# Kernel tuning notes

Measured on AMD Instinct MI355X. Metric: run time of the kernel, lower is better.

Reference implementation:

```python
import jax, jax.numpy as jnp
import numpy as np

S, B, H, NH = 2048, 1, 4096, 32
HD = H // NH            # 128
ROT = int(HD * 0.25)    # 32 partial rotary dims
BASE = 10000.0


def setup_inputs() -> dict:
    key = jax.random.key(0)
    ks = jax.random.split(key, 4)
    hidden_states = jax.random.normal(ks[0], (S, B, H), dtype=jnp.float32)
    W_qkv = jax.random.normal(ks[1], (3 * H, H), dtype=jnp.float32) * 0.02
    b_qkv = jnp.zeros((3 * H,), dtype=jnp.float32)
    W_dense = jax.random.normal(ks[2], (H, H), dtype=jnp.float32) * 0.02
    b_dense = jnp.zeros((H,), dtype=jnp.float32)
    # causal left-to-right mask, True = attend
    attention_mask = jnp.tril(jnp.ones((S, S), dtype=bool))[None, None]  # [1,1,S,S]
    return dict(hidden_states=hidden_states, attention_mask=attention_mask,
                W_qkv=W_qkv, b_qkv=b_qkv, W_dense=W_dense, b_dense=b_dense)


def _rotate_half(x):
    x1, x2 = jnp.split(x, 2, axis=-1)
    return jnp.concatenate((-x2, x1), axis=-1)


def reference(hidden_states, attention_mask, W_qkv, b_qkv, W_dense, b_dense):
    S_, B_ = hidden_states.shape[:2]
    qkv = hidden_states @ W_qkv.T + b_qkv                    # [S,B,3H]
    qkv = qkv.reshape(S_, B_, NH, 3 * HD)
    q, k, v = qkv[..., :HD], qkv[..., HD:2 * HD], qkv[..., 2 * HD:]

    # partial rotary embedding (GPT-NeoX style, offset=0, no KV cache)
    inv_freq = 1.0 / (BASE ** (jnp.arange(0, ROT, 2, dtype=jnp.float32) / ROT))
    t = jnp.arange(S_, dtype=jnp.float32)
    freqs = jnp.einsum('s,d->sd', t, inv_freq)               # [S,ROT/2]
    emb = jnp.concatenate((freqs, freqs), axis=-1)           # [S,ROT]
    cos = jnp.cos(emb)[:, None, None, :]                     # [S,1,1,ROT]
    sin = jnp.sin(emb)[:, None, None, :]

    def rope(x):
        return x * cos + _rotate_half(x) * sin

    q = jnp.concatenate((rope(q[..., :ROT]), q[..., ROT:]), axis=-1)
    k = jnp.concatenate((rope(k[..., :ROT]), k[..., ROT:]), axis=-1)

    # scaled dot-product attention with explicit score matrix
    scores = jnp.einsum('sbhd,tbhd->bhst', q, k) / np.float32(np.sqrt(HD))
    scores = jnp.where(attention_mask, scores, jnp.float32(-10000.0))
    probs = jax.nn.softmax(scores, axis=-1)                  # [B,NH,S,S]
    ctx = jnp.einsum('bhst,tbhd->sbhd', probs, v).reshape(S_, B_, H)
    return ctx @ W_dense.T + b_dense                         # [S,B,H]
```

## Files before the change

### kernel.cpp

```cpp
#include <hip/hip_runtime.h>
#include <hip/hip_bf16.h>

typedef __bf16 bf16_t;
typedef bf16_t bf16x8 __attribute__((ext_vector_type(8)));
typedef bf16_t bf16x4 __attribute__((ext_vector_type(4)));
typedef float floatx4 __attribute__((ext_vector_type(4)));

#define S_LEN 2048
#define NHEADS 32
#define HD 128
#define QKV_LD 12288

__global__ void f32_to_bf16_k(const float* __restrict__ in, bf16_t* __restrict__ out, int n4) {
    int i = blockIdx.x * 256 + threadIdx.x;
    if (i >= n4) return;
    float4 v = ((const float4*)in)[i];
    bf16x4 o;
    o.x = (bf16_t)v.x; o.y = (bf16_t)v.y; o.z = (bf16_t)v.z; o.w = (bf16_t)v.w;
    ((bf16x4*)out)[i] = o;
}

__device__ __forceinline__ void async_copy16(const void* g, void* l) {
    __builtin_amdgcn_global_load_lds(
        (const __attribute__((address_space(1))) unsigned int*)g,
        (__attribute__((address_space(3))) unsigned int*)l, 16, 0, 0);
}

template<bool OUT_BF16>
__global__ __launch_bounds__(256) void gemm_bt(
    const bf16_t* __restrict__ A, const bf16_t* __restrict__ B,
    const float* __restrict__ bias, void* __restrict__ Cv,
    int M, int N, int K)
{
    __shared__ bf16_t As[128 * 32];
    __shared__ bf16_t Bs[128 * 32];
    const int t    = threadIdx.x;
    const int lane = t & 63;
    const int w    = t >> 6;
    const int l15  = lane & 15;
    const int quad = lane >> 4;
    const int bm = blockIdx.y, bn = blockIdx.x;
    const int mw = (w >> 1) * 64, nw = (w & 1) * 64;

    floatx4 acc[4][4];
    #pragma unroll
    for (int i = 0; i < 4; i++)
        #pragma unroll
        for (int j = 0; j < 4; j++)
            acc[i][j] = (floatx4){0.f, 0.f, 0.f, 0.f};

    const int r0 = t >> 2;
    const int c0 = (t & 3) * 8;
    const bf16_t* Aptr = A + (size_t)(bm * 128 + r0) * K + c0;
    const bf16_t* Bptr = B + (size_t)(bn * 128 + r0) * K + c0;
    bf16_t* AsW = As + t * 8;
    bf16_t* BsW = Bs + t * 8;

    for (int k0 = 0; k0 < K; k0 += 32) {
        __syncthreads();
        async_copy16(Aptr + k0, AsW);
        async_copy16(Aptr + k0 + (size_t)64 * K, AsW + 2048);
        async_copy16(Bptr + k0, BsW);
        async_copy16(Bptr + k0 + (size_t)64 * K, BsW + 2048);
        __syncthreads();

        bf16x8 a[4], b[4];
        #pragma unroll
        for (int mi = 0; mi < 4; mi++)
            a[mi] = *(const bf16x8*)&As[(mw + mi * 16 + l15) * 32 + quad * 8];
        #pragma unroll
        for (int ni = 0; ni < 4; ni++)
            b[ni] = *(const bf16x8*)&Bs[(nw + ni * 16 + l15) * 32 + quad * 8];
        #pragma unroll
        for (int mi = 0; mi < 4; mi++)
            #pragma unroll
            for (int ni = 0; ni < 4; ni++)
                acc[mi][ni] = __builtin_amdgcn_mfma_f32_16x16x32_bf16(a[mi], b[ni], acc[mi][ni], 0, 0, 0);
    }

    float bv[4];
    #pragma unroll
    for (int ni = 0; ni < 4; ni++)
        bv[ni] = bias[bn * 128 + nw + ni * 16 + l15];
    #pragma unroll
    for (int mi = 0; mi < 4; mi++) {
        #pragma unroll
        for (int ni = 0; ni < 4; ni++) {
            int col = bn * 128 + nw + ni * 16 + l15;
            #pragma unroll
            for (int r = 0; r < 4; r++) {
                int row = bm * 128 + mw + mi * 16 + quad * 4 + r;
                float v = acc[mi][ni][r] + bv[ni];
                if (OUT_BF16)
                    ((bf16_t*)Cv)[(size_t)row * N + col] = (bf16_t)v;
                else
                    ((float*)Cv)[(size_t)row * N + col] = v;
            }
        }
    }
}

__global__ void rope_kernel(bf16_t* __restrict__ qkv) {
    int idx = blockIdx.x * 256 + threadIdx.x;
    int j = idx & 15;
    int h = (idx >> 4) & 31;
    int s = idx >> 9;
    float freq = (float)s * powf(10000.f, -(float)j / 16.f);
    float sn, cs;
    sincosf(freq, &sn, &cs);
    bf16_t* base = qkv + (size_t)s * QKV_LD + h * 384;
    {
        float x1 = (float)base[j], x2 = (float)base[j + 16];
        base[j]      = (bf16_t)(x1 * cs - x2 * sn);
        base[j + 16] = (bf16_t)(x2 * cs + x1 * sn);
    }
    {
        bf16_t* kb = base + 128;
        float x1 = (float)kb[j], x2 = (float)kb[j + 16];
        kb[j]      = (bf16_t)(x1 * cs - x2 * sn);
        kb[j + 16] = (bf16_t)(x2 * cs + x1 * sn);
    }
}

__global__ void vtrans_kernel(const bf16_t* __restrict__ qkv, bf16_t* __restrict__ Vt) {
    __shared__ bf16_t tile[64][68];
    int h = blockIdx.y;
    int stile = blockIdx.x >> 1, dtile = blockIdx.x & 1;
    int t = threadIdx.x;
    int tr = t >> 4;
    int tc4 = (t & 15) * 4;
    const bf16_t* src = qkv + (size_t)(stile * 64) * QKV_LD + h * 384 + 256 + dtile * 64;
    #pragma unroll
    for (int r = 0; r < 4; r++) {
        int srow = tr + r * 16;
        *(bf16x4*)&tile[srow][tc4] = *(const bf16x4*)&src[(size_t)srow * QKV_LD + tc4];
    }
    __syncthreads();
    bf16_t* dst = Vt + ((size_t)h * HD + dtile * 64) * S_LEN + stile * 64;
    #pragma unroll
    for (int r = 0; r < 4; r++) {
        int drow = tr + r * 16;
        bf16x4 v;
        #pragma unroll
        for (int j = 0; j < 4; j++) v[j] = tile[tc4 + j][drow];
        *(bf16x4*)&dst[(size_t)drow * S_LEN + tc4] = v;
    }
}

#define QK_LDS 136
#define V_LDS  72
__global__ __launch_bounds__(256) void flash_attn(
    const bf16_t* __restrict__ qkv, const bf16_t* __restrict__ Vt,
    bf16_t* __restrict__ ctx)
{
    __shared__ bf16_t Qs[64 * QK_LDS];
    __shared__ bf16_t Ks[64 * QK_LDS];
    __shared__ bf16_t Vs[128 * V_LDS];
    __shared__ bf16_t Ps[64 * V_LDS];
    const int h = blockIdx.y;
    const int qb = blockIdx.x;
    const int t = threadIdx.x;
    const int w = t >> 6, lane = t & 63;
    const int quad = lane >> 4, l15 = lane & 15;
    const float L2E = 1.4426950408889634f;
    const float ISQ = 0.08838834764831845f;

    {
        const bf16_t* qbase = qkv + (size_t)(qb * 64) * QKV_LD + h * 384;
        int rr = t >> 4, cc = (t & 15) * 8;
        #pragma unroll
        for (int p = 0; p < 4; p++) {
            int row = rr + p * 16;
            *(bf16x8*)&Qs[row * QK_LDS + cc] = *(const bf16x8*)&qbase[(size_t)row * QKV_LD + cc];
        }
    }

    floatx4 o[8];
    #pragma unroll
    for (int i = 0; i < 8; i++) o[i] = (floatx4){0.f, 0.f, 0.f, 0.f};
    float mrow[4] = {-1e30f, -1e30f, -1e30f, -1e30f};
    float lrow[4] = {0.f, 0.f, 0.f, 0.f};

    for (int kt = 0; kt <= qb; kt++) {
        __syncthreads();
        {
            const bf16_t* kbase = qkv + (size_t)(kt * 64) * QKV_LD + h * 384 + 128;
            int rr = t >> 4, cc = (t & 15) * 8;
            #pragma unroll
            for (int p = 0; p < 4; p++) {
                int row = rr + p * 16;
                *(bf16x8*)&Ks[row * QK_LDS + cc] = *(const bf16x8*)&kbase[(size_t)row * QKV_LD + cc];
            }
            const bf16_t* vbase = Vt + (size_t)h * HD * S_LEN + kt * 64;
            int vr = t >> 3, vc = (t & 7) * 8;
            #pragma unroll
            for (int p = 0; p < 4; p++) {
                int row = vr + p * 32;
                *(bf16x8*)&Vs[row * V_LDS + vc] = *(const bf16x8*)&vbase[(size_t)row * S_LEN + vc];
            }
        }
        __syncthreads();

        floatx4 sacc[4];
        #pragma unroll
        for (int ni = 0; ni < 4; ni++) sacc[ni] = (floatx4){0.f, 0.f, 0.f, 0.f};
        #pragma unroll
        for (int ks = 0; ks < 4; ks++) {
            bf16x8 aq = *(const bf16x8*)&Qs[(w * 16 + l15) * QK_LDS + ks * 32 + quad * 8];
            #pragma unroll
            for (int ni = 0; ni < 4; ni++) {
                bf16x8 bk = *(const bf16x8*)&Ks[(ni * 16 + l15) * QK_LDS + ks * 32 + quad * 8];
                sacc[ni] = __builtin_amdgcn_mfma_f32_16x16x32_bf16(aq, bk, sacc[ni], 0, 0, 0);
            }
        }

        float p_[4][4];
        #pragma unroll
        for (int ni = 0; ni < 4; ni++)
            #pragma unroll
            for (int r = 0; r < 4; r++)
                p_[ni][r] = sacc[ni][r] * ISQ;
        if (kt == qb) {
            #pragma unroll
            for (int ni = 0; ni < 4; ni++) {
                int key = ni * 16 + l15;
                #pragma unroll
                for (int r = 0; r < 4; r++)
                    if (key > w * 16 + quad * 4 + r) p_[ni][r] = -1e30f;
            }
        }

        float alpha[4];
        #pragma unroll
        for (int r = 0; r < 4; r++) {
            float mx = fmaxf(fmaxf(p_[0][r], p_[1][r]), fmaxf(p_[2][r], p_[3][r]));
            #pragma unroll
            for (int off = 1; off < 16; off <<= 1)
                mx = fmaxf(mx, __shfl_xor(mx, off, 16));
            float mnew = fmaxf(mrow[r], mx);
            alpha[r] = __builtin_amdgcn_exp2f((mrow[r] - mnew) * L2E);
            mrow[r] = mnew;
        }
        float lad[4] = {0.f, 0.f, 0.f, 0.f};
        #pragma unroll
        for (int ni = 0; ni < 4; ni++)
            #pragma unroll
            for (int r = 0; r < 4; r++) {
                float pv = __builtin_amdgcn_exp2f((p_[ni][r] - mrow[r]) * L2E);
                p_[ni][r] = pv;
                lad[r] += pv;
            }
        #pragma unroll
        for (int r = 0; r < 4; r++) {
            #pragma unroll
            for (int off = 1; off < 16; off <<= 1)
                lad[r] += __shfl_xor(lad[r], off, 16);
            lrow[r] = lrow[r] * alpha[r] + lad[r];
        }
        #pragma unroll
        for (int ni = 0; ni < 8; ni++)
            #pragma unroll
            for (int r = 0; r < 4; r++)
                o[ni][r] *= alpha[r];

        #pragma unroll
        for (int ni = 0; ni < 4; ni++)
            #pragma unroll
            for (int r = 0; r < 4; r++)
                Ps[(w * 16 + quad * 4 + r) * V_LDS + ni * 16 + l15] = (bf16_t)p_[ni][r];
        __syncthreads();

        #pragma unroll
        for (int ks = 0; ks < 2; ks++) {
            bf16x8 ap = *(const bf16x8*)&Ps[(w * 16 + l15) * V_LDS + ks * 32 + quad * 8];
            #pragma unroll
            for (int ni = 0; ni < 8; ni++) {
                bf16x8 bv = *(const bf16x8*)&Vs[(ni * 16 + l15) * V_LDS + ks * 32 + quad * 8];
                o[ni] = __builtin_amdgcn_mfma_f32_16x16x32_bf16(ap, bv, o[ni], 0, 0, 0);
            }
        }
    }

    float invl[4];
    #pragma unroll
    for (int r = 0; r < 4; r++) invl[r] = 1.f / lrow[r];
    bf16_t* cbase = ctx + (size_t)(qb * 64) * 4096 + h * HD;
    #pragma unroll
    for (int ni = 0; ni < 8; ni++) {
        int col = ni * 16 + l15;
        #pragma unroll
        for (int r = 0; r < 4; r++) {
            int row = w * 16 + quad * 4 + r;
            cbase[(size_t)row * 4096 + col] = (bf16_t)(o[ni][r] * invl[r]);
        }
    }
}

extern "C" void kernel_launch(void* const* d_in, const int* in_sizes, int n_in,
                              void* d_out, int out_size, void* d_ws, size_t ws_size,
                              hipStream_t stream) {
    const float* hidden = (const float*)d_in[0];
    const float* Wqkv   = (const float*)d_in[2];
    const float* bqkv   = (const float*)d_in[3];
    const float* Wd     = (const float*)d_in[4];
    const float* bd     = (const float*)d_in[5];
    float* out = (float*)d_out;

    char* ws = (char*)d_ws;
    bf16_t* h_bf    = (bf16_t*)(ws);
    bf16_t* wqkv_bf = (bf16_t*)(ws + 16777216);
    bf16_t* wd_bf   = (bf16_t*)(ws + 117440512);
    bf16_t* qkv     = (bf16_t*)(ws + 150994944);
    bf16_t* vt      = (bf16_t*)(ws + 201326592);
    bf16_t* ctx     = (bf16_t*)(ws + 218103808);

    f32_to_bf16_k<<<8192,  256, 0, stream>>>(hidden, h_bf,    2097152);
    f32_to_bf16_k<<<49152, 256, 0, stream>>>(Wqkv,   wqkv_bf, 12582912);
    f32_to_bf16_k<<<16384, 256, 0, stream>>>(Wd,     wd_bf,   4194304);

    gemm_bt<true><<<dim3(96, 16), 256, 0, stream>>>(h_bf, wqkv_bf, bqkv, qkv, 2048, 12288, 4096);
    rope_kernel<<<4096, 256, 0, stream>>>(qkv);
    vtrans_kernel<<<dim3(64, 32), 256, 0, stream>>>(qkv, vt);
    flash_attn<<<dim3(32, 32), 256, 0, stream>>>(qkv, vt, ctx);
    gemm_bt<false><<<dim3(32, 16), 256, 0, stream>>>(ctx, wd_bf, bd, out, 2048, 4096, 4096);
}
```

Before: 929.2 us.

## Fuse RoPE and V transpose into QKV GEMM epilogue, merge conversions

Folds the rotary embedding and the V transpose into the QKV GEMM epilogue. Q/K go to a compact buffer and V is written already transposed, which removes two separate kernels and their global round trips. The three fp32-to-bf16 conversions become one launch. Flash attention now schedules the heaviest causal query blocks first, and the barrier after writing P is replaced with an LDS waitcnt, which relies on each wave only reading its own P rows.

Measured after the change: 933.6 us. About the same (+0.5%).

```diff
diff --git a/kernel.cpp b/kernel.cpp
--- a/kernel.cpp
+++ b/kernel.cpp
@@ -1,5 +1,6 @@
 #include <hip/hip_runtime.h>
 #include <hip/hip_bf16.h>
+#include <math.h>
 
 typedef __bf16 bf16_t;
 typedef bf16_t bf16x8 __attribute__((ext_vector_type(8)));
@@ -7,17 +8,20 @@
 typedef float floatx4 __attribute__((ext_vector_type(4)));
 
 #define S_LEN 2048
-#define NHEADS 32
-#define HD 128
-#define QKV_LD 12288
-
-__global__ void f32_to_bf16_k(const float* __restrict__ in, bf16_t* __restrict__ out, int n4) {
+#define QK_LD 8192
+
+__global__ void convert_all(const float* __restrict__ a, bf16_t* __restrict__ ao,
+                            const float* __restrict__ b, bf16_t* __restrict__ bo,
+                            const float* __restrict__ c, bf16_t* __restrict__ co) {
     int i = blockIdx.x * 256 + threadIdx.x;
-    if (i >= n4) return;
-    float4 v = ((const float4*)in)[i];
+    const float* src; bf16_t* dst; int j;
+    if (i < 2097152)        { src = a; dst = ao; j = i; }
+    else if (i < 14680064)  { src = b; dst = bo; j = i - 2097152; }
+    else                    { src = c; dst = co; j = i - 14680064; }
+    float4 v = ((const float4*)src)[j];
     bf16x4 o;
     o.x = (bf16_t)v.x; o.y = (bf16_t)v.y; o.z = (bf16_t)v.z; o.w = (bf16_t)v.w;
-    ((bf16x4*)out)[i] = o;
+    ((bf16x4*)dst)[j] = o;
 }
 
 __device__ __forceinline__ void async_copy16(const void* g, void* l) {
@@ -26,10 +30,116 @@
         (__attribute__((address_space(3))) unsigned int*)l, 16, 0, 0);
 }
 
-template<bool OUT_BF16>
-__global__ __launch_bounds__(256) void gemm_bt(
+__global__ __launch_bounds__(256) void qkv_gemm(
     const bf16_t* __restrict__ A, const bf16_t* __restrict__ B,
-    const float* __restrict__ bias, void* __restrict__ Cv,
+    const float* __restrict__ bias, bf16_t* __restrict__ qkout,
+    bf16_t* __restrict__ vt)
+{
+    __shared__ bf16_t As[128 * 32];
+    __shared__ bf16_t Bs[128 * 32];
+    const int K = 4096;
+    const int t    = threadIdx.x;
+    const int lane = t & 63;
+    const int w    = t >> 6;
+    const int l15  = lane & 15;
+    const int quad = lane >> 4;
+    const int bm = blockIdx.y, bn = blockIdx.x;
+    const int mw = (w >> 1) * 64, nw = (w & 1) * 64;
+
+    floatx4 acc[4][4];
+    #pragma unroll
+    for (int i = 0; i < 4; i++)
+        #pragma unroll
+        for (int j = 0; j < 4; j++)
+            acc[i][j] = (floatx4){0.f, 0.f, 0.f, 0.f};
+
+    const int r0 = t >> 2;
+    const int c0 = (t & 3) * 8;
+    const bf16_t* Aptr = A + (size_t)(bm * 128 + r0) * K + c0;
+    const bf16_t* Bptr = B + (size_t)(bn * 128 + r0) * K + c0;
+    bf16_t* AsW = As + t * 8;
+    bf16_t* BsW = Bs + t * 8;
+
+    for (int k0 = 0; k0 < K; k0 += 32) {
+        __syncthreads();
+        async_copy16(Aptr + k0, AsW);
+        async_copy16(Aptr + k0 + (size_t)64 * K, AsW + 2048);
+        async_copy16(Bptr + k0, BsW);
+        async_copy16(Bptr + k0 + (size_t)64 * K, BsW + 2048);
+        __syncthreads();
+
+        bf16x8 a[4], b[4];
+        #pragma unroll
+        for (int mi = 0; mi < 4; mi++)
+            a[mi] = *(const bf16x8*)&As[(mw + mi * 16 + l15) * 32 + quad * 8];
+        #pragma unroll
+        for (int ni = 0; ni < 4; ni++)
+            b[ni] = *(const bf16x8*)&Bs[(nw + ni * 16 + l15) * 32 + quad * 8];
+        #pragma unroll
+        for (int mi = 0; mi < 4; mi++)
+            #pragma unroll
+            for (int ni = 0; ni < 4; ni++)
+                acc[mi][ni] = __builtin_amdgcn_mfma_f32_16x16x32_bf16(a[mi], b[ni], acc[mi][ni], 0, 0, 0);
+    }
+
+    #pragma unroll
+    for (int ni = 0; ni < 4; ni++) {
+        float bv = bias[bn * 128 + nw + ni * 16 + l15];
+        #pragma unroll
+        for (int mi = 0; mi < 4; mi++)
+            #pragma unroll
+            for (int r = 0; r < 4; r++)
+                acc[mi][ni][r] += bv;
+    }
+
+    const int h = bn / 3, ht = bn - h * 3;
+    if (ht < 2) {
+        if (nw == 0) {
+            float invf = exp2f(-(float)l15 * 0.8304820237218405f);
+            #pragma unroll
+            for (int mi = 0; mi < 4; mi++)
+                #pragma unroll
+                for (int r = 0; r < 4; r++) {
+                    int s = bm * 128 + mw + mi * 16 + quad * 4 + r;
+                    float sn, cs;
+                    sincosf((float)s * invf, &sn, &cs);
+                    float x1 = acc[mi][0][r], x2 = acc[mi][1][r];
+                    acc[mi][0][r] = x1 * cs - x2 * sn;
+                    acc[mi][1][r] = x2 * cs + x1 * sn;
+                }
+        }
+        bf16_t* base = qkout + h * 256 + ht * 128;
+        #pragma unroll
+        for (int mi = 0; mi < 4; mi++)
+            #pragma unroll
+            for (int ni = 0; ni < 4; ni++) {
+                int col = nw + ni * 16 + l15;
+                #pragma unroll
+                for (int r = 0; r < 4; r++) {
+                    int row = bm * 128 + mw + mi * 16 + quad * 4 + r;
+                    base[(size_t)row * QK_LD + col] = (bf16_t)acc[mi][ni][r];
+                }
+            }
+    } else {
+        bf16_t* vbase = vt + (size_t)h * 128 * S_LEN;
+        #pragma unroll
+        for (int mi = 0; mi < 4; mi++) {
+            int s0 = bm * 128 + mw + mi * 16 + quad * 4;
+            #pragma unroll
+            for (int ni = 0; ni < 4; ni++) {
+                int d = nw + ni * 16 + l15;
+                bf16x4 pv;
+                #pragma unroll
+                for (int r = 0; r < 4; r++) pv[r] = (bf16_t)acc[mi][ni][r];
+                *(bf16x4*)&vbase[(size_t)d * S_LEN + s0] = pv;
+            }
+        }
+    }
+}
+
+__global__ __launch_bounds__(256) void dense_gemm(
+    const bf16_t* __restrict__ A, const bf16_t* __restrict__ B,
+    const float* __restrict__ bias, float* __restrict__ C,
     int M, int N, int K)
 {
     __shared__ bf16_t As[128 * 32];
@@ -78,79 +188,24 @@
                 acc[mi][ni] = __builtin_amdgcn_mfma_f32_16x16x32_bf16(a[mi], b[ni], acc[mi][ni], 0, 0, 0);
     }
 
-    float bv[4];
-    #pragma unroll
-    for (int ni = 0; ni < 4; ni++)
-        bv[ni] = bias[bn * 128 + nw + ni * 16 + l15];
-    #pragma unroll
-    for (int mi = 0; mi < 4; mi++) {
-        #pragma unroll
-        for (int ni = 0; ni < 4; ni++) {
-            int col = bn * 128 + nw + ni * 16 + l15;
+    #pragma unroll
+    for (int ni = 0; ni < 4; ni++) {
+        float bv = bias[bn * 128 + nw + ni * 16 + l15];
+        int col = bn * 128 + nw + ni * 16 + l15;
+        #pragma unroll
+        for (int mi = 0; mi < 4; mi++)
             #pragma unroll
             for (int r = 0; r < 4; r++) {
                 int row = bm * 128 + mw + mi * 16 + quad * 4 + r;
-                float v = acc[mi][ni][r] + bv[ni];
-                if (OUT_BF16)
-                    ((bf16_t*)Cv)[(size_t)row * N + col] = (bf16_t)v;
-                else
-                    ((float*)Cv)[(size_t)row * N + col] = v;
-            }
-        }
-    }
-}
-
-__global__ void rope_kernel(bf16_t* __restrict__ qkv) {
-    int idx = blockIdx.x * 256 + threadIdx.x;
-    int j = idx & 15;
-    int h = (idx >> 4) & 31;
-    int s = idx >> 9;
-    float freq = (float)s * powf(10000.f, -(float)j / 16.f);
-    float sn, cs;
-    sincosf(freq, &sn, &cs);
-    bf16_t* base = qkv + (size_t)s * QKV_LD + h * 384;
-    {
-        float x1 = (float)base[j], x2 = (float)base[j + 16];
-        base[j]      = (bf16_t)(x1 * cs - x2 * sn);
-        base[j + 16] = (bf16_t)(x2 * cs + x1 * sn);
-    }
-    {
-        bf16_t* kb = base + 128;
-        float x1 = (float)kb[j], x2 = (float)kb[j + 16];
-        kb[j]      = (bf16_t)(x1 * cs - x2 * sn);
-        kb[j + 16] = (bf16_t)(x2 * cs + x1 * sn);
-    }
-}
-
-__global__ void vtrans_kernel(const bf16_t* __restrict__ qkv, bf16_t* __restrict__ Vt) {
-    __shared__ bf16_t tile[64][68];
-    int h = blockIdx.y;
-    int stile = blockIdx.x >> 1, dtile = blockIdx.x & 1;
-    int t = threadIdx.x;
-    int tr = t >> 4;
-    int tc4 = (t & 15) * 4;
-    const bf16_t* src = qkv + (size_t)(stile * 64) * QKV_LD + h * 384 + 256 + dtile * 64;
-    #pragma unroll
-    for (int r = 0; r < 4; r++) {
-        int srow = tr + r * 16;
-        *(bf16x4*)&tile[srow][tc4] = *(const bf16x4*)&src[(size_t)srow * QKV_LD + tc4];
-    }
-    __syncthreads();
-    bf16_t* dst = Vt + ((size_t)h * HD + dtile * 64) * S_LEN + stile * 64;
-    #pragma unroll
-    for (int r = 0; r < 4; r++) {
-        int drow = tr + r * 16;
-        bf16x4 v;
-        #pragma unroll
-        for (int j = 0; j < 4; j++) v[j] = tile[tc4 + j][drow];
-        *(bf16x4*)&dst[(size_t)drow * S_LEN + tc4] = v;
+                C[(size_t)row * N + col] = acc[mi][ni][r] + bv;
+            }
     }
 }
 
 #define QK_LDS 136
 #define V_LDS  72
 __global__ __launch_bounds__(256) void flash_attn(
-    const bf16_t* __restrict__ qkv, const bf16_t* __restrict__ Vt,
+    const bf16_t* __restrict__ qk, const bf16_t* __restrict__ Vt,
     bf16_t* __restrict__ ctx)
 {
     __shared__ bf16_t Qs[64 * QK_LDS];
@@ -158,7 +213,7 @@
     __shared__ bf16_t Vs[128 * V_LDS];
     __shared__ bf16_t Ps[64 * V_LDS];
     const int h = blockIdx.y;
-    const int qb = blockIdx.x;
+    const int qb = (int)gridDim.x - 1 - blockIdx.x;
     const int t = threadIdx.x;
     const int w = t >> 6, lane = t & 63;
     const int quad = lane >> 4, l15 = lane & 15;
@@ -166,12 +221,12 @@
     const float ISQ = 0.08838834764831845f;
 
     {
-        const bf16_t* qbase = qkv + (size_t)(qb * 64) * QKV_LD + h * 384;
+        const bf16_t* qbase = qk + (size_t)(qb * 64) * QK_LD + h * 256;
         int rr = t >> 4, cc = (t & 15) * 8;
         #pragma unroll
         for (int p = 0; p < 4; p++) {
             int row = rr + p * 16;
-            *(bf16x8*)&Qs[row * QK_LDS + cc] = *(const bf16x8*)&qbase[(size_t)row * QKV_LD + cc];
+            *(bf16x8*)&Qs[row * QK_LDS + cc] = *(const bf16x8*)&qbase[(size_t)row * QK_LD + cc];
         }
     }
 
@@ -184,14 +239,14 @@
     for (int kt = 0; kt <= qb; kt++) {
         __syncthreads();
         {
-            const bf16_t* kbase = qkv + (size_t)(kt * 64) * QKV_LD + h * 384 + 128;
+            const bf16_t* kbase = qk + (size_t)(kt * 64) * QK_LD + h * 256 + 128;
             int rr = t >> 4, cc = (t & 15) * 8;
             #pragma unroll
             for (int p = 0; p < 4; p++) {
                 int row = rr + p * 16;
-                *(bf16x8*)&Ks[row * QK_LDS + cc] = *(const bf16x8*)&kbase[(size_t)row * QKV_LD + cc];
-            }
-            const bf16_t* vbase = Vt + (size_t)h * HD * S_LEN + kt * 64;
+                *(bf16x8*)&Ks[row * QK_LDS + cc] = *(const bf16x8*)&kbase[(size_t)row * QK_LD + cc];
+            }
+            const bf16_t* vbase = Vt + (size_t)h * 128 * S_LEN + kt * 64;
             int vr = t >> 3, vc = (t & 7) * 8;
             #pragma unroll
             for (int p = 0; p < 4; p++) {
@@ -268,7 +323,7 @@
             #pragma unroll
             for (int r = 0; r < 4; r++)
                 Ps[(w * 16 + quad * 4 + r) * V_LDS + ni * 16 + l15] = (bf16_t)p_[ni][r];
-        __syncthreads();
+        asm volatile("s_waitcnt lgkmcnt(0)" ::: "memory");
 
         #pragma unroll
         for (int ks = 0; ks < 2; ks++) {
@@ -284,7 +339,7 @@
     float invl[4];
     #pragma unroll
     for (int r = 0; r < 4; r++) invl[r] = 1.f / lrow[r];
-    bf16_t* cbase = ctx + (size_t)(qb * 64) * 4096 + h * HD;
+    bf16_t* cbase = ctx + (size_t)(qb * 64) * 4096 + h * 128;
     #pragma unroll
     for (int ni = 0; ni < 8; ni++) {
         int col = ni * 16 + l15;
@@ -310,17 +365,12 @@
     bf16_t* h_bf    = (bf16_t*)(ws);
     bf16_t* wqkv_bf = (bf16_t*)(ws + 16777216);
     bf16_t* wd_bf   = (bf16_t*)(ws + 117440512);
-    bf16_t* qkv     = (bf16_t*)(ws + 150994944);
-    bf16_t* vt      = (bf16_t*)(ws + 201326592);
-    bf16_t* ctx     = (bf16_t*)(ws + 218103808);
-
-    f32_to_bf16_k<<<8192,  256, 0, stream>>>(hidden, h_bf,    2097152);
-    f32_to_bf16_k<<<49152, 256, 0, stream>>>(Wqkv,   wqkv_bf, 12582912);
-    f32_to_bf16_k<<<16384, 256, 0, stream>>>(Wd,     wd_bf,   4194304);
-
-    gemm_bt<true><<<dim3(96, 16), 256, 0, stream>>>(h_bf, wqkv_bf, bqkv, qkv, 2048, 12288, 4096);
-    rope_kernel<<<4096, 256, 0, stream>>>(qkv);
-    vtrans_kernel<<<dim3(64, 32), 256, 0, stream>>>(qkv, vt);
-    flash_attn<<<dim3(32, 32), 256, 0, stream>>>(qkv, vt, ctx);
-    gemm_bt<false><<<dim3(32, 16), 256, 0, stream>>>(ctx, wd_bf, bd, out, 2048, 4096, 4096);
-}
+    bf16_t* qk      = (bf16_t*)(ws + 150994944);
+    bf16_t* vt      = (bf16_t*)(ws + 184549376);
+    bf16_t* ctx     = (bf16_t*)(ws + 201326592);
+
+    convert_all<<<73728, 256, 0, stream>>>(hidden, h_bf, Wqkv, wqkv_bf, Wd, wd_bf);
+    qkv_gemm<<<dim3(96, 16), 256, 0, stream>>>(h_bf, wqkv_bf, bqkv, qk, vt);
+    flash_attn<<<dim3(32, 32), 256, 0, stream>>>(qk, vt, ctx);
+    dense_gemm<<<dim3(32, 16), 256, 0, stream>>>(ctx, wd_bf, bd, out, 2048, 4096, 4096);
+}
```
